# Optimization experiments

Measured on AMD Instinct MI355X. Metric: run time of the kernel, lower is better.

## Reference

```python
import jax, jax.numpy as jnp
import numpy as np

G_GRAPHS = 10000
K = 17  # keypoints per graph
# COCO-17 skeleton bones
SKEL = np.array([(15,13),(13,11),(16,14),(14,12),(11,12),(5,11),(6,12),(5,6),(5,7),
                 (6,8),(7,9),(8,10),(1,2),(0,1),(0,2),(1,3),(2,4),(3,5),(4,6)], dtype=np.int64)
DIMS = [2, 64, 64, 64, 128, 128, 128, 256, 256, 256]
BN_EPS = 1e-5


def setup_inputs() -> dict:
    key = jax.random.key(0)
    ks = jax.random.split(key, 16)
    N = G_GRAPHS * K
    # per-graph skeleton edges (bidirectional), offset per graph
    e = np.concatenate([SKEL, SKEL[:, ::-1]], axis=0)            # [38,2]
    off = np.arange(G_GRAPHS, dtype=np.int64)[:, None, None] * K
    edges = (e[None, :, :] + off).reshape(-1, 2)                 # [G*38, 2]
    inp = {
        'x': jax.random.normal(ks[0], (N, 2), jnp.float32),
        'att': jax.random.uniform(ks[1], (N, 1), jnp.float32),
        'edge_index': jnp.asarray(edges.T),                      # [2, E] int64->int32 ok
    }
    for i in range(9):
        kw = jax.random.fold_in(ks[2], i)
        scale = 1.0 / np.sqrt(DIMS[i])
        inp[f'W{i+1}'] = (jax.random.normal(kw, (DIMS[i], DIMS[i+1]), jnp.float32) * scale)
        inp[f'b{i+1}'] = jnp.zeros((DIMS[i+1],), jnp.float32)
    inp['fcW'] = jax.random.normal(ks[3], (6, 256, 256), jnp.float32) * (1.0 / 16.0)  # [scale,out,in]
    inp['fcB'] = jnp.zeros((6, 256), jnp.float32)
    inp['bn_gamma'] = jnp.ones((6, 256), jnp.float32)
    inp['bn_beta'] = jnp.zeros((6, 256), jnp.float32)
    inp['bn_rm'] = jnp.zeros((6, 256), jnp.float32)
    inp['bn_rv'] = jnpp if False else jnp.ones((6, 256), jnp.float32)
    return inp


def _forward(x, att, edge_index, Ws, bs, fcW, fcB, bn_gamma, bn_beta, bn_rm, bn_rv):
    N = x.shape[0]
    ar = jnp.arange(N, dtype=edge_index.dtype)
    src = jnp.concatenate([edge_index[0], ar])   # add self-loops (PyG GCNConv default)
    dst = jnp.concatenate([edge_index[1], ar])
    deg = jax.ops.segment_sum(jnp.ones_like(dst, dtype=jnp.float32), dst, num_segments=N)
    dinv = 1.0 / jnp.sqrt(deg)                   # deg >= 1 due to self-loops
    norm = (dinv[src] * dinv[dst])[:, None]      # [E+N, 1]

    h = x
    for W, b in zip(Ws, bs):
        msg = (h @ W)[src] * norm                # gather-linear-scale
        agg = jax.ops.segment_sum(msg, dst, num_segments=N)
        h = jnp.maximum((agg + b) * att, 0.0)    # AttGCNConv * att, then ReLU

    # JRPP pooling: [B, 17, 256] -> [B, 6, 256]
    xg = h.reshape(-1, K, h.shape[-1])
    g1 = xg.mean(axis=1, keepdims=True)
    g2 = jnp.concatenate([xg[:, :11].mean(1, keepdims=True),
                          xg[:, 11:].mean(1, keepdims=True)], axis=1)
    head = xg[:, jnp.array([0, 1, 2, 3, 4])].mean(1, keepdims=True)
    larl = xg[:, jnp.array([5, 7, 9, 12, 14, 16])].mean(1, keepdims=True)
    rall = xg[:, jnp.array([6, 8, 10, 11, 13, 15])].mean(1, keepdims=True)
    pooled = jnp.concatenate([g1, g2, head, larl, rall], axis=1)  # [B, 6, 256]

    # per-scale Linear (torch weight layout [out,in]) + eval-mode BatchNorm1d
    ft = jnp.einsum('bsi,soi->bso', pooled, fcW) + fcB
    fi = (ft - bn_rm) * (bn_gamma / jnp.sqrt(bn_rv + BN_EPS)) + bn_beta
    out = fi.reshape(fi.shape[0], -1)            # [B, 1536]
    # F.normalize(p=2, dim=1)
    nrm = jnp.maximum(jnp.linalg.norm(out, axis=1, keepdims=True), 1e-12)
    return out / nrm


def reference(x, att, edge_index, W1, b1, W2, b2, W3, b3, W4, b4, W5, b5, W6, b6,
              W7, b7, W8, b8, W9, b9, fcW, fcB, bn_gamma, bn_beta, bn_rm, bn_rv):
    Ws = [W1, W2, W3, W4, W5, W6, W7, W8, W9]
    bs = [b1, b2, b3, b4, b5, b6, b7, b8, b9]
    return _forward(x, att, edge_index, Ws, bs, fcW, fcB, bn_gamma, bn_beta, bn_rm, bn_rv)
```

## Files before the change

### kernel.cpp

```cpp
#include <hip/hip_runtime.h>
#include <math.h>


typedef _Float16 f16;
typedef _Float16 v2h __attribute__((ext_vector_type(2)));
typedef _Float16 v4h __attribute__((ext_vector_type(4)));
typedef _Float16 v8h __attribute__((ext_vector_type(8)));
typedef float    v4f __attribute__((ext_vector_type(4)));

namespace {

constexpr int BA[19] = {15,13,16,14,11, 5, 6, 5, 5, 6, 7, 8, 1, 0, 0, 1, 2, 3, 4};
constexpr int BB[19] = {13,11,14,12,12,11,12, 6, 7, 8, 9,10, 2, 1, 2, 3, 4, 5, 6};
constexpr float DINV[17] = {
  0.57735026919f, 0.5f, 0.5f, 0.57735026919f, 0.57735026919f,
  0.44721359550f, 0.44721359550f, 0.57735026919f, 0.57735026919f,
  0.70710678119f, 0.70710678119f, 0.5f, 0.5f,
  0.57735026919f, 0.57735026919f, 0.70710678119f, 0.70710678119f};

__device__ __forceinline__ int hswz(int row, int k){
  return row*256 + (k & ~63) + (((((k>>3)&7) ^ (row&7)))<<3) + (k&7);
}
__device__ __forceinline__ int zswz(int c, int r){
  return c*64 + (r ^ ((c&7)<<3));
}

__device__ __forceinline__ void ldh2(const f16* p, float* d){
  const v2h v = *(const v2h*)p; d[0]=v[0]; d[1]=v[1];
}

template<int KP, int DOUT>
__device__ __forceinline__ void layer_phase(const f16* __restrict__ src,
    f16* __restrict__ dst, f16* ztw,
    const f16* __restrict__ wp, const float* __restrict__ bias,
    const float (&av3)[3], const v8h (&Bfrag)[3][2],
    int w, int m, int q)
{
  constexpr int NKS = KP/32;
  constexpr int NTW = DOUT/64;
  constexpr int CT_PER = (NTW>=2)?2:1;
  constexpr int NPASS = NTW/CT_PER;

  v4f acc[3][NTW];
  #pragma unroll
  for (int a=0;a<3;++a)
    #pragma unroll
    for (int b=0;b<NTW;++b) acc[a][b] = v4f{0.f,0.f,0.f,0.f};

  #pragma unroll
  for (int ks=0; ks<NKS; ++ks){
    v8h af[3];
    #pragma unroll
    for (int mt=0;mt<3;++mt)
      af[mt] = *(const v8h*)(src + hswz(mt*16+m, ks*32 + q*8));
    #pragma unroll
    for (int nt=0;nt<NTW;++nt){
      const v8h bf = *(const v8h*)(wp + ((((w*NTW+nt)*NKS + ks)*64 + q*16 + m)<<3));
      #pragma unroll
      for (int mt=0;mt<3;++mt)
        acc[mt][nt] = __builtin_amdgcn_mfma_f32_16x16x32_f16(af[mt], bf, acc[mt][nt], 0,0,0);
    }
  }

  #pragma unroll
  for (int p=0;p<NPASS;++p){
    #pragma unroll
    for (int nt2=0;nt2<CT_PER;++nt2){
      #pragma unroll
      for (int mt=0;mt<3;++mt){
        v4h z;
        #pragma unroll
        for (int ii=0;ii<4;++ii) z[ii] = (f16)acc[mt][p*CT_PER+nt2][ii];
        *(v4h*)(ztw + zswz(nt2*16+m, mt*16+q*4)) = z;
      }
    }
    #pragma unroll
    for (int ct2=0;ct2<CT_PER;++ct2){
      const v8h za0 = *(const v8h*)(ztw + zswz(ct2*16+m, q*8));
      const v8h za1 = *(const v8h*)(ztw + zswz(ct2*16+m, 32 + q*8));
      v4f a2[3];
      #pragma unroll
      for (int mt=0;mt<3;++mt) a2[mt] = v4f{0.f,0.f,0.f,0.f};
      #pragma unroll
      for (int mt=0;mt<3;++mt)
        a2[mt] = __builtin_amdgcn_mfma_f32_16x16x32_f16(za0, Bfrag[mt][0], a2[mt], 0,0,0);
      #pragma unroll
      for (int mt=0;mt<3;++mt)
        a2[mt] = __builtin_amdgcn_mfma_f32_16x16x32_f16(za1, Bfrag[mt][1], a2[mt], 0,0,0);
      const int cb = w*(DOUT/4) + (p*CT_PER+ct2)*16 + q*4;
      const v4f b4 = *(const v4f*)(bias + cb);
      #pragma unroll
      for (int mt=0;mt<3;++mt){
        v4h o;
        #pragma unroll
        for (int ii=0;ii<4;++ii)
          o[ii] = (f16)fmaxf((a2[mt][ii] + b4[ii])*av3[mt], 0.f);
        *(v4h*)(dst + hswz(mt*16+m, cb)) = o;
      }
    }
  }
}

}

__global__ void prep_kernel(
    const float* __restrict__ W1, const float* __restrict__ W2,
    const float* __restrict__ W3, const float* __restrict__ W4,
    const float* __restrict__ W5, const float* __restrict__ W6,
    const float* __restrict__ W7, const float* __restrict__ W8,
    const float* __restrict__ W9,
    const float* __restrict__ B1, const float* __restrict__ B2,
    const float* __restrict__ B3, const float* __restrict__ B4,
    const float* __restrict__ B5, const float* __restrict__ B6,
    const float* __restrict__ B7, const float* __restrict__ B8,
    const float* __restrict__ B9,
    const float* __restrict__ fcW, const float* __restrict__ bng,
    const float* __restrict__ bnb, const float* __restrict__ bnrm,
    const float* __restrict__ bnrv, const float* __restrict__ att,
    f16* __restrict__ wt, f16* __restrict__ Ath, f16* __restrict__ fcWh,
    float* __restrict__ bnsc, float* __restrict__ bnsh,
    float* __restrict__ bcat, float* __restrict__ attp, int G)
{
  const int idx = blockIdx.x*blockDim.x + threadIdx.x;
  const int stride = gridDim.x*blockDim.x;
  const float* Ws[9] = {W1,W2,W3,W4,W5,W6,W7,W8,W9};
  const float* Bs[9] = {B1,B2,B3,B4,B5,B6,B7,B8,B9};
  const int DINs[9]  = {2,64,64,64,128,128,128,256,256};
  const int DOUTs[9] = {64,64,64,128,128,128,256,256,256};
  const int KPs[9]   = {32,64,64,64,128,128,128,256,256};
  const int OFFs[9]  = {0,2048,6144,10240,18432,34816,51200,83968,149504};
  const int BOFFs[9] = {0,64,128,192,320,448,576,832,1088};
  for (int l=0;l<9;++l){
    const float* W = Ws[l];
    const int DIN=DINs[l], DOUT=DOUTs[l], KP=KPs[l], NKS=KP>>5;
    f16* dst = wt + OFFs[l];
    const int n = DOUT*KP;
    for (int i=idx;i<n;i+=stride){
      const int jj = i&7, mm = (i>>3)&15, qq = (i>>7)&3, r2 = i>>9;
      const int ks = r2 & (NKS-1), ct = r2 / NKS;
      const int k = ks*32 + qq*8 + jj, c = ct*16 + mm;
      dst[i] = (k<DIN) ? (f16)W[k*DOUT + c] : (f16)0.f;
    }
    for (int i=idx;i<DOUT;i+=stride) bcat[BOFFs[l]+i] = Bs[l][i];
  }
  for (int i=idx;i<48*64;i+=stride){
    const int r = i>>6, j = i&63;
    float v = 0.f;
    if (j < 48 && ((r<24) == (j<24))){
      const int a = (r<24)? r : r-24;
      const int b = (j<24)? j : j-24;
      if (a<17 && b<17){
        bool adj = (a==b);
        #pragma unroll
        for (int e=0;e<19;++e)
          adj = adj || (BA[e]==a && BB[e]==b) || (BA[e]==b && BB[e]==a);
        if (adj) v = DINV[a]*DINV[b];
      }
    }
    Ath[i] = (f16)v;
  }
  for (int i=idx;i<6*256*256;i+=stride) fcWh[i] = (f16)fcW[i];
  for (int i=idx;i<1536;i+=stride){
    const float sc = bng[i] * rsqrtf(bnrv[i] + 1e-5f);
    bnsc[i] = sc; bnsh[i] = bnb[i] - bnrm[i]*sc;
  }
  const int G2 = (G+1)&~1;
  for (int i=idx;i<G2*24;i+=stride){
    const int g = i/24, j = i - g*24;
    attp[i] = (j<17 && g<G) ? att[(size_t)g*17 + j] : 0.f;
  }
}

__global__ __launch_bounds__(256, 2)
void gcn_kernel(const float* __restrict__ x, const f16* __restrict__ wt,
                const f16* __restrict__ Ath, const float* __restrict__ attp,
                const float* __restrict__ bcat,
                f16* __restrict__ pooled, int G)
{
  __shared__ __align__(16) f16 Hb[2][48*256];
  __shared__ __align__(16) f16 Zt[4*2048];
  const int t = threadIdx.x, w = t>>6, lane = t&63;
  const int m = lane&15, q = lane>>4;
  const int g0 = blockIdx.x*2;
  f16* ztw = Zt + w*2048;

  v8h Bfrag[3][2];
  #pragma unroll
  for (int mt=0;mt<3;++mt)
    #pragma unroll
    for (int ks2=0;ks2<2;++ks2)
      Bfrag[mt][ks2] = *(const v8h*)(Ath + (mt*16+m)*64 + ks2*32 + q*8);
  float av3[3];
  #pragma unroll
  for (int mt=0;mt<3;++mt) av3[mt] = attp[g0*24 + mt*16 + m];

  {
    const v8h z8 = {0,0,0,0,0,0,0,0};
    #pragma unroll
    for (int i=0;i<4;++i) *(v8h*)(Zt + t*32 + i*8) = z8;
    const int g = t>>7, kk = t&127;
    if (kk < 32){
      #pragma unroll
      for (int i=0;i<17;++i){
        float v = 0.f;
        if (kk < 2 && g0+g < G) v = x[(size_t)(g0+g)*34 + i*2 + kk];
        Hb[0][hswz(g*24+i, kk)] = (f16)v;
      }
      #pragma unroll
      for (int j=17;j<24;++j) Hb[0][hswz(g*24+j, kk)] = (f16)0.f;
    }
  }
  __syncthreads();

  layer_phase< 32, 64>(Hb[0], Hb[1], ztw, wt+0,      bcat+0,    av3, Bfrag, w, m, q); __syncthreads();
  layer_phase< 64, 64>(Hb[1], Hb[0], ztw, wt+2048,   bcat+64,   av3, Bfrag, w, m, q); __syncthreads();
  layer_phase< 64, 64>(Hb[0], Hb[1], ztw, wt+6144,   bcat+128,  av3, Bfrag, w, m, q); __syncthreads();
  layer_phase< 64,128>(Hb[1], Hb[0], ztw, wt+10240,  bcat+192,  av3, Bfrag, w, m, q); __syncthreads();
  layer_phase<128,128>(Hb[0], Hb[1], ztw, wt+18432,  bcat+320,  av3, Bfrag, w, m, q); __syncthreads();
  layer_phase<128,128>(Hb[1], Hb[0], ztw, wt+34816,  bcat+448,  av3, Bfrag, w, m, q); __syncthreads();
  layer_phase<128,256>(Hb[0], Hb[1], ztw, wt+51200,  bcat+576,  av3, Bfrag, w, m, q); __syncthreads();
  layer_phase<256,256>(Hb[1], Hb[0], ztw, wt+83968,  bcat+832,  av3, Bfrag, w, m, q); __syncthreads();
  layer_phase<256,256>(Hb[0], Hb[1], ztw, wt+149504, bcat+1088, av3, Bfrag, w, m, q); __syncthreads();

  const int g = t>>7, tt = t&127, k0 = tt*2, gg = g0 + g;
  if (gg < G){
    float sA[2]={0,0}, sB[2]={0,0}, sH[2]={0,0}, sL[2]={0,0}, sR[2]={0,0};
    #pragma unroll
    for (int i=0;i<17;++i){
      float hi[2];
      ldh2(&Hb[1][hswz(g*24+i, k0)], hi);
      #pragma unroll
      for (int v=0;v<2;++v){
        if (i<11) sA[v]+=hi[v]; else sB[v]+=hi[v];
        if (i<5)  sH[v]+=hi[v];
        if (i==5||i==7||i==9||i==12||i==14||i==16)  sL[v]+=hi[v];
        if (i==6||i==8||i==10||i==11||i==13||i==15) sR[v]+=hi[v];
      }
    }
    f16* op = pooled + (size_t)gg*1536 + k0;
    v2h o;
    #pragma unroll
    for (int v=0;v<2;++v) o[v]=(f16)((sA[v]+sB[v])*(1.0f/17.0f)); *(v2h*)(op+0*256)=o;
    #pragma unroll
    for (int v=0;v<2;++v) o[v]=(f16)(sA[v]*(1.0f/11.0f));         *(v2h*)(op+1*256)=o;
    #pragma unroll
    for (int v=0;v<2;++v) o[v]=(f16)(sB[v]*(1.0f/6.0f));          *(v2h*)(op+2*256)=o;
    #pragma unroll
    for (int v=0;v<2;++v) o[v]=(f16)(sH[v]*(1.0f/5.0f));          *(v2h*)(op+3*256)=o;
    #pragma unroll
    for (int v=0;v<2;++v) o[v]=(f16)(sL[v]*(1.0f/6.0f));          *(v2h*)(op+4*256)=o;
    #pragma unroll
    for (int v=0;v<2;++v) o[v]=(f16)(sR[v]*(1.0f/6.0f));          *(v2h*)(op+5*256)=o;
  }
}

__global__ __launch_bounds__(256, 2)
void head_kernel(const f16* __restrict__ pooled, const f16* __restrict__ fcWh,
                 const float* __restrict__ fcB, const float* __restrict__ bnsc,
                 const float* __restrict__ bnsh, float* __restrict__ out, int G)
{
  __shared__ __align__(16) f16 Ap[16*1536];
  __shared__ float red[64];
  __shared__ float invn[16];
  const int t = threadIdx.x, w = t>>6, lane = t&63;
  const int m = lane&15, q = lane>>4;
  const int g0 = blockIdx.x*16;
  const int cb = w*64;

  for (int id=t; id<16*192; id+=256){
    const int row = id/192, cc = id - row*192;
    v8h v = v8h{0,0,0,0,0,0,0,0};
    const int gg = g0 + row;
    if (gg < G) v = *(const v8h*)(pooled + (size_t)gg*1536 + cc*8);
    const int pc = (cc & ~7) | ((cc&7) ^ (row&7));
    *(v8h*)(Ap + row*1536 + pc*8) = v;
  }
  __syncthreads();

  v4f acc[6][4];
  #pragma unroll
  for (int s=0;s<6;++s)
    #pragma unroll
    for (int nt=0;nt<4;++nt) acc[s][nt] = v4f{0.f,0.f,0.f,0.f};

  #pragma unroll
  for (int s=0;s<6;++s){
    #pragma unroll
    for (int ks=0; ks<8; ++ks){
      const int c = s*32 + ks*4 + q;
      const v8h af = *(const v8h*)(Ap + m*1536 + ((c & ~7) | ((c&7) ^ (m&7)))*8);
      #pragma unroll
      for (int nt=0;nt<4;++nt){
        const v8h bf = *(const v8h*)(fcWh + (size_t)(s*256 + cb + nt*16 + m)*256 + ks*32 + q*8);
        acc[s][nt] = __builtin_amdgcn_mfma_f32_16x16x32_f16(af, bf, acc[s][nt], 0,0,0);
      }
    }
  }

  float ss[4] = {0.f,0.f,0.f,0.f};
  #pragma unroll
  for (int s=0;s<6;++s)
    #pragma unroll
    for (int nt=0;nt<4;++nt){
      const int idx = s*256 + cb + nt*16 + m;
      const float bc = fcB[idx], sc = bnsc[idx], sh = bnsh[idx];
      #pragma unroll
      for (int i=0;i<4;++i){
        const float f = (acc[s][nt][i] + bc)*sc + sh;
        acc[s][nt][i] = f;
        ss[i] += f*f;
      }
    }

  #pragma unroll
  for (int off=1; off<16; off<<=1)
    #pragma unroll
    for (int i=0;i<4;++i) ss[i] += __shfl_xor(ss[i], off, 64);
  if (m==0)
    #pragma unroll
    for (int i=0;i<4;++i) red[w*16 + q*4 + i] = ss[i];
  __syncthreads();
  if (t < 16){
    const float s4 = red[t] + red[16+t] + red[32+t] + red[48+t];
    invn[t] = 1.f / fmaxf(sqrtf(s4), 1e-12f);
  }
  __syncthreads();
  float iv[4];
  #pragma unroll
  for (int i=0;i<4;++i) iv[i] = invn[q*4+i];
  #pragma unroll
  for (int s=0;s<6;++s)
    #pragma unroll
    for (int nt=0;nt<4;++nt)
      #pragma unroll
      for (int i=0;i<4;++i){
        const int gg = g0 + q*4 + i;
        if (gg < G)
          out[(size_t)gg*1536 + s*256 + cb + nt*16 + m] = acc[s][nt][i]*iv[i];
      }
}

extern "C" void kernel_launch(void* const* d_in, const int* in_sizes, int n_in,
                              void* d_out, int out_size, void* d_ws, size_t ws_size,
                              hipStream_t stream) {
  (void)n_in; (void)out_size; (void)ws_size;
  const float* x   = (const float*)d_in[0];
  const float* att = (const float*)d_in[1];
  const float* W[9]; const float* B[9];
  for (int i=0;i<9;i++){ W[i]=(const float*)d_in[3+2*i]; B[i]=(const float*)d_in[4+2*i]; }
  const float* fcW  = (const float*)d_in[21];
  const float* fcB  = (const float*)d_in[22];
  const float* bn_g = (const float*)d_in[23];
  const float* bn_b = (const float*)d_in[24];
  const float* bn_rm= (const float*)d_in[25];
  const float* bn_rv= (const float*)d_in[26];
  float* out = (float*)d_out;

  const int G = in_sizes[1] / 17;
  const int G2 = (G+1)&~1;

  char* ws = (char*)d_ws;
  f16*   wt   = (f16*)(ws);
  f16*   fcWh = (f16*)(ws + 430080);
  float* bnsc = (float*)(ws + 1216512);
  float* bnsh = (float*)(ws + 1222656);
  float* bcat = (float*)(ws + 1228800);
  f16*   Ath  = (f16*)(ws + 1234176);
  float* attp = (float*)(ws + 1240320);
  size_t poolOff = (1240320 + (size_t)G2*96 + 255) & ~(size_t)255;
  f16* pooled = (f16*)(ws + poolOff);

  prep_kernel<<<256, 256, 0, stream>>>(
      W[0],W[1],W[2],W[3],W[4],W[5],W[6],W[7],W[8],
      B[0],B[1],B[2],B[3],B[4],B[5],B[6],B[7],B[8],
      fcW, bn_g, bn_b, bn_rm, bn_rv, att,
      wt, Ath, fcWh, bnsc, bnsh, bcat, attp, G);

  const int gb = (G + 1) / 2;
  gcn_kernel<<<gb, 256, 0, stream>>>(
      x, wt, Ath, attp, bcat, pooled, G);

  head_kernel<<<(G + 15)/16, 256, 0, stream>>>(
      pooled, fcWh, fcB, bnsc, bnsh, out, G);
}
```

Measured before the change: 378.0 us.

## Update layer activations in place in one LDS buffer to raise occupancy

Replaces the ping-pong pair of shared-memory activation buffers with a single buffer that each layer updates in place. A block barrier is inserted between the MFMA reads of the input tile and the epilogue writes of the output tile so no wave overwrites rows another wave still needs. This cuts per-block LDS use so more blocks can be resident per CU, and launch bounds are raised to 4 blocks per multiprocessor to match. The cost is one extra barrier per layer and a tighter register budget, which could cause spills in the wide 256-column layers.

```diff
diff --git a/kernel.cpp b/kernel.cpp
--- a/kernel.cpp
+++ b/kernel.cpp
@@ -30,8 +30,7 @@
 }
 
 template<int KP, int DOUT>
-__device__ __forceinline__ void layer_phase(const f16* __restrict__ src,
-    f16* __restrict__ dst, f16* ztw,
+__device__ __forceinline__ void layer_phase(f16* __restrict__ H, f16* ztw,
     const f16* __restrict__ wp, const float* __restrict__ bias,
     const float (&av3)[3], const v8h (&Bfrag)[3][2],
     int w, int m, int q)
@@ -52,7 +51,7 @@
     v8h af[3];
     #pragma unroll
     for (int mt=0;mt<3;++mt)
-      af[mt] = *(const v8h*)(src + hswz(mt*16+m, ks*32 + q*8));
+      af[mt] = *(const v8h*)(H + hswz(mt*16+m, ks*32 + q*8));
     #pragma unroll
     for (int nt=0;nt<NTW;++nt){
       const v8h bf = *(const v8h*)(wp + ((((w*NTW+nt)*NKS + ks)*64 + q*16 + m)<<3));
@@ -61,6 +60,8 @@
         acc[mt][nt] = __builtin_amdgcn_mfma_f32_16x16x32_f16(af[mt], bf, acc[mt][nt], 0,0,0);
     }
   }
+
+  __syncthreads();
 
   #pragma unroll
   for (int p=0;p<NPASS;++p){
@@ -95,7 +96,7 @@
         #pragma unroll
         for (int ii=0;ii<4;++ii)
           o[ii] = (f16)fmaxf((a2[mt][ii] + b4[ii])*av3[mt], 0.f);
-        *(v4h*)(dst + hswz(mt*16+m, cb)) = o;
+        *(v4h*)(H + hswz(mt*16+m, cb)) = o;
       }
     }
   }
@@ -171,13 +172,13 @@
   }
 }
 
-__global__ __launch_bounds__(256, 2)
+__global__ __launch_bounds__(256, 4)
 void gcn_kernel(const float* __restrict__ x, const f16* __restrict__ wt,
                 const f16* __restrict__ Ath, const float* __restrict__ attp,
                 const float* __restrict__ bcat,
                 f16* __restrict__ pooled, int G)
 {
-  __shared__ __align__(16) f16 Hb[2][48*256];
+  __shared__ __align__(16) f16 Hb[48*256];
   __shared__ __align__(16) f16 Zt[4*2048];
   const int t = threadIdx.x, w = t>>6, lane = t&63;
   const int m = lane&15, q = lane>>4;
@@ -204,23 +205,23 @@
       for (int i=0;i<17;++i){
         float v = 0.f;
         if (kk < 2 && g0+g < G) v = x[(size_t)(g0+g)*34 + i*2 + kk];
-        Hb[0][hswz(g*24+i, kk)] = (f16)v;
-      }
-      #pragma unroll
-      for (int j=17;j<24;++j) Hb[0][hswz(g*24+j, kk)] = (f16)0.f;
-    }
-  }
-  __syncthreads();
-
-  layer_phase< 32, 64>(Hb[0], Hb[1], ztw, wt+0,      bcat+0,    av3, Bfrag, w, m, q); __syncthreads();
-  layer_phase< 64, 64>(Hb[1], Hb[0], ztw, wt+2048,   bcat+64,   av3, Bfrag, w, m, q); __syncthreads();
-  layer_phase< 64, 64>(Hb[0], Hb[1], ztw, wt+6144,   bcat+128,  av3, Bfrag, w, m, q); __syncthreads();
-  layer_phase< 64,128>(Hb[1], Hb[0], ztw, wt+10240,  bcat+192,  av3, Bfrag, w, m, q); __syncthreads();
-  layer_phase<128,128>(Hb[0], Hb[1], ztw, wt+18432,  bcat+320,  av3, Bfrag, w, m, q); __syncthreads();
-  layer_phase<128,128>(Hb[1], Hb[0], ztw, wt+34816,  bcat+448,  av3, Bfrag, w, m, q); __syncthreads();
-  layer_phase<128,256>(Hb[0], Hb[1], ztw, wt+51200,  bcat+576,  av3, Bfrag, w, m, q); __syncthreads();
-  layer_phase<256,256>(Hb[1], Hb[0], ztw, wt+83968,  bcat+832,  av3, Bfrag, w, m, q); __syncthreads();
-  layer_phase<256,256>(Hb[0], Hb[1], ztw, wt+149504, bcat+1088, av3, Bfrag, w, m, q); __syncthreads();
+        Hb[hswz(g*24+i, kk)] = (f16)v;
+      }
+      #pragma unroll
+      for (int j=17;j<24;++j) Hb[hswz(g*24+j, kk)] = (f16)0.f;
+    }
+  }
+  __syncthreads();
+
+  layer_phase< 32, 64>(Hb, ztw, wt+0,      bcat+0,    av3, Bfrag, w, m, q); __syncthreads();
+  layer_phase< 64, 64>(Hb, ztw, wt+2048,   bcat+64,   av3, Bfrag, w, m, q); __syncthreads();
+  layer_phase< 64, 64>(Hb, ztw, wt+6144,   bcat+128,  av3, Bfrag, w, m, q); __syncthreads();
+  layer_phase< 64,128>(Hb, ztw, wt+10240,  bcat+192,  av3, Bfrag, w, m, q); __syncthreads();
+  layer_phase<128,128>(Hb, ztw, wt+18432,  bcat+320,  av3, Bfrag, w, m, q); __syncthreads();
+  layer_phase<128,128>(Hb, ztw, wt+34816,  bcat+448,  av3, Bfrag, w, m, q); __syncthreads();
+  layer_phase<128,256>(Hb, ztw, wt+51200,  bcat+576,  av3, Bfrag, w, m, q); __syncthreads();
+  layer_phase<256,256>(Hb, ztw, wt+83968,  bcat+832,  av3, Bfrag, w, m, q); __syncthreads();
+  layer_phase<256,256>(Hb, ztw, wt+149504, bcat+1088, av3, Bfrag, w, m, q); __syncthreads();
 
   const int g = t>>7, tt = t&127, k0 = tt*2, gg = g0 + g;
   if (gg < G){
@@ -228,7 +229,7 @@
     #pragma unroll
     for (int i=0;i<17;++i){
       float hi[2];
-      ldh2(&Hb[1][hswz(g*24+i, k0)], hi);
+      ldh2(&Hb[hswz(g*24+i, k0)], hi);
       #pragma unroll
       for (int v=0;v<2;++v){
         if (i<11) sA[v]+=hi[v]; else sB[v]+=hi[v];
```

Measured after the change: 444.6 us. 17.6% more time.
